# Kernel tuning notes

Hardware: AMD Instinct MI355X
Metric: run time of the kernel (lower is better)

The kernel has to match this reference:

```python
import jax, jax.numpy as jnp
import numpy as np

V, E, H = 512, 128, 256
B, S, T = 2048, 32, 48


def setup_inputs() -> dict:
    key = jax.random.key(0)
    ks = jax.random.split(key, 13)
    def p(i, shape):
        return jax.random.normal(ks[i], shape, dtype=jnp.float32) * 0.05
    return {
        "source": jax.random.randint(ks[0], (B, S), 0, V),
        "target_len": T,
        "enc_emb": p(1, (V, E)),
        "enc_Wih": p(2, (4 * H, E)),
        "enc_Whh": p(3, (4 * H, H)),
        "enc_bih": p(4, (4 * H,)),
        "enc_bhh": p(5, (4 * H,)),
        "dec_emb": p(6, (V, E)),
        "dec_Wih": p(7, (4 * H, E)),
        "dec_Whh": p(8, (4 * H, H)),
        "dec_bih": p(9, (4 * H,)),
        "dec_bhh": p(10, (4 * H,)),
        "fc_W": p(11, (V, H)),
        "fc_b": p(12, (V,)),
    }


def lstm_cell(x, h, c, Wih, Whh, bih, bhh):
    # torch gate order: i, f, g, o
    z = x @ Wih.T + h @ Whh.T + (bih + bhh)
    i, f, g, o = jnp.split(z, 4, axis=-1)
    c = jax.nn.sigmoid(f) * c + jax.nn.sigmoid(i) * jnp.tanh(g)
    h = jax.nn.sigmoid(o) * jnp.tanh(c)
    return h, c


def reference(source, target_len, enc_emb, enc_Wih, enc_Whh, enc_bih, enc_bhh,
              dec_emb, dec_Wih, dec_Whh, dec_bih, dec_bhh, fc_W, fc_b):
    Bsz = source.shape[0]
    Hd = enc_Whh.shape[1]
    h0 = jnp.zeros((Bsz, Hd), dtype=enc_emb.dtype)
    c0 = jnp.zeros((Bsz, Hd), dtype=enc_emb.dtype)

    # ---- encoder: embed whole source, scan single-layer LSTM over time ----
    emb_seq = jnp.swapaxes(enc_emb[source], 0, 1)  # [S, B, E]

    def enc_step(carry, x_t):
        h, c = carry
        h, c = lstm_cell(x_t, h, c, enc_Wih, enc_Whh, enc_bih, enc_bhh)
        return (h, c), None

    (h, c), _ = jax.lax.scan(enc_step, (h0, c0), emb_seq)

    sos = jnp.zeros((Bsz,), dtype=jnp.int32)  # char2idx.get('<SOS>', 0) == 0

    def dec_step(carry, _):
        tok, h, c = carry
        x = dec_emb[tok]                         # [B, E]
        h, c = lstm_cell(x, h, c, dec_Wih, dec_Whh, dec_bih, dec_bhh)
        logits = h @ fc_W.T + fc_b               # [B, V]
        nxt = jnp.argmax(logits, axis=-1).astype(jnp.int32)
        return (nxt, h, c), logits

    _, logits = jax.lax.scan(dec_step, (sos, h, c), None, length=target_len)
    return jnp.swapaxes(logits, 0, 1)            # [B, target_len, V]
```

## Files before the change

kernel.cpp:

```cpp
#include <hip/hip_runtime.h>
#include <cmath>

#define S_LEN 32
#define E_DIM 128
#define H_DIM 256
#define V_DIM 512
#define NTILE 12
#define W_TILES 8
#define TILE_SHORTS 8192
#define A_SHORTS 8192
#define ZPITCH 132

typedef _Float16 f16x8v __attribute__((ext_vector_type(8)));
typedef float f32x16 __attribute__((ext_vector_type(16)));

#define SCALE_S 4096.0f
#define INV_S   2.44140625e-4f

__device__ __forceinline__ float sigf(float x) { return 1.0f / (1.0f + expf(-x)); }

template<int L>
__device__ __forceinline__ unsigned short lvl_f16(float x) {
  _Float16 h1 = (_Float16)x;
  if (L == 1) return __builtin_bit_cast(unsigned short, h1);
  _Float16 h2 = (_Float16)((x - (float)h1) * SCALE_S);
  return __builtin_bit_cast(unsigned short, h2);
}

__global__ void prep_weights(const float* __restrict__ eemb, const float* __restrict__ demb,
                             const float* __restrict__ eWih, const float* __restrict__ eWhh,
                             const float* __restrict__ dWih, const float* __restrict__ dWhh,
                             unsigned short* __restrict__ We, unsigned short* __restrict__ Wd,
                             float* __restrict__ PE, float* __restrict__ PD,
                             float* __restrict__ h0, float* __restrict__ c,
                             int* __restrict__ tok)
{
  const int b = blockIdx.x;
  if (b >= 1152) {
    const int pb = b - 1152;
    const int gt = pb * 256 + threadIdx.x;
    float4 z = make_float4(0.f, 0.f, 0.f, 0.f);
    float4* p0 = (float4*)h0;
    float4* pc = (float4*)c;
    for (int i = gt; i < 131072; i += 16384) { p0[i] = z; pc[i] = z; }
    if (gt < 2048) tok[gt] = 0;
    return;
  }
  if (b >= 128) {
    const int pb  = b - 128;
    const int set = pb >> 9;
    const int v   = pb & 511;
    const float* Wih  = set ? dWih : eWih;
    const float* embr = (set ? demb : eemb) + (size_t)v * E_DIM;
    float* dst = (set ? PD : PE) + (size_t)v * 1024;
    const int n0 = threadIdx.x * 4;
    float acc[4] = {0.f, 0.f, 0.f, 0.f};
    #pragma unroll 4
    for (int k0 = 0; k0 < E_DIM; k0 += 4) {
      float4 e = *(const float4*)(embr + k0);
      #pragma unroll
      for (int i = 0; i < 4; ++i) {
        float4 wv = *(const float4*)(Wih + (size_t)(n0 + i) * E_DIM + k0);
        acc[i] = fmaf(e.x, wv.x, acc[i]);
        acc[i] = fmaf(e.y, wv.y, acc[i]);
        acc[i] = fmaf(e.z, wv.z, acc[i]);
        acc[i] = fmaf(e.w, wv.w, acc[i]);
      }
    }
    *(float4*)(dst + n0) = make_float4(acc[0], acc[1], acc[2], acc[3]);
    return;
  }
  const int j    = b % W_TILES;
  const int rest = b / W_TILES;
  const int nb   = rest & 7;
  const int set  = rest >> 3;
  const float* Whh = set ? dWhh : eWhh;
  unsigned short* dst = (set ? Wd : We) + ((size_t)nb * W_TILES + j) * TILE_SHORTS;
  const int lvl = (j < 4) ? 1 : 2;
  const int jj  = j & 3;

  for (int cpos = threadIdx.x; cpos < 1024; cpos += 256) {
    int fi = cpos >> 6, l = cpos & 63;
    int g = fi >> 2, kc = fi & 3;
    int n  = g * H_DIM + nb * 32 + (l & 31);
    int kk = jj * 64 + kc * 16 + (l >> 5) * 8;
    unsigned short o8[8];
    #pragma unroll
    for (int e = 0; e < 8; ++e) {
      float v = Whh[(size_t)n * H_DIM + kk + e];
      o8[e] = (lvl == 1) ? lvl_f16<1>(v) : lvl_f16<2>(v);
    }
    uint4 pk;
    pk.x = (unsigned)o8[0] | ((unsigned)o8[1] << 16);
    pk.y = (unsigned)o8[2] | ((unsigned)o8[3] << 16);
    pk.z = (unsigned)o8[4] | ((unsigned)o8[5] << 16);
    pk.w = (unsigned)o8[6] | ((unsigned)o8[7] << 16);
    *(uint4*)&dst[(size_t)cpos * 8] = pk;
  }
}

__device__ __forceinline__ void stage_A12(unsigned short* Ax1, unsigned short* Ax2,
                                          const float* __restrict__ hsrc,
                                          int arow, int q8) {
  #pragma unroll
  for (int j = 0; j < 8; ++j) {
    int kA = q8 * 4 + 32 * j;
    float4 v = *(const float4*)(hsrc + kA);
    _Float16 a1x = (_Float16)v.x, a1y = (_Float16)v.y,
             a1z = (_Float16)v.z, a1w = (_Float16)v.w;
    _Float16 a2x = (_Float16)((v.x - (float)a1x) * SCALE_S);
    _Float16 a2y = (_Float16)((v.y - (float)a1y) * SCALE_S);
    _Float16 a2z = (_Float16)((v.z - (float)a1z) * SCALE_S);
    _Float16 a2w = (_Float16)((v.w - (float)a1w) * SCALE_S);
    int lane_w = arow + ((kA >> 3) & 1) * 32;
    int idx = ((kA >> 4) * 64 + lane_w) * 8 + (kA & 7);
    uint2 p1, p2;
    p1.x = (unsigned)__builtin_bit_cast(unsigned short, a1x)
         | ((unsigned)__builtin_bit_cast(unsigned short, a1y) << 16);
    p1.y = (unsigned)__builtin_bit_cast(unsigned short, a1z)
         | ((unsigned)__builtin_bit_cast(unsigned short, a1w) << 16);
    p2.x = (unsigned)__builtin_bit_cast(unsigned short, a2x)
         | ((unsigned)__builtin_bit_cast(unsigned short, a2y) << 16);
    p2.y = (unsigned)__builtin_bit_cast(unsigned short, a2z)
         | ((unsigned)__builtin_bit_cast(unsigned short, a2w) << 16);
    *(uint2*)&Ax1[idx] = p1;
    *(uint2*)&Ax2[idx] = p2;
  }
}

__launch_bounds__(256, 2)
__global__ void lstm_mfma_kernel(const float* __restrict__ pcomp,
                                 const int* __restrict__ idx_src, int idx_stride, int idx_off,
                                 const unsigned short* __restrict__ Wf,
                                 const float* __restrict__ bih, const float* __restrict__ bhh,
                                 const float* __restrict__ h_in,
                                 float* __restrict__ h_out, float* __restrict__ c)
{
  __shared__ __align__(16) unsigned short smem[2 * A_SHORTS];
  unsigned short* Ax1 = smem;
  unsigned short* Ax2 = smem + A_SHORTS;

  const int tid  = threadIdx.x;
  const int lane = tid & 63;
  const int w    = tid >> 6;
  const int m0 = blockIdx.x * 32;
  const int nb = blockIdx.y;
  const int nc0 = nb * 32;

  const int arow = tid >> 3;
  const int q8   = tid & 7;
  const int token = idx_src[(size_t)(m0 + arow) * idx_stride + idx_off];
  const float* hsrc = h_in + (size_t)(m0 + arow) * H_DIM;

  const int col32 = lane & 31;
  const int lhi   = lane >> 5;

  const unsigned short* wbase = Wf + (size_t)nb * (W_TILES * TILE_SHORTS)
                                   + (size_t)(w * 4) * 512 + (size_t)lane * 8;

  f32x16 accA, accB;
  #pragma unroll
  for (int r = 0; r < 16; ++r) { accA[r] = 0.f; accB[r] = 0.f; }

  uint4 pA[4], pB[4], pC[4], pD[4];

#define LOADT(J, P)                                                            \
  {                                                                            \
    const unsigned short* bsrc = wbase + (size_t)((J) & 7) * TILE_SHORTS;      \
    _Pragma("unroll")                                                          \
    for (int kc = 0; kc < 4; ++kc) P[kc] = *(const uint4*)(bsrc + (size_t)kc * 512); \
  }

#define MFMAT(J, P, ACCX, AXB)                                                 \
  {                                                                            \
    _Pragma("unroll")                                                          \
    for (int kc = 0; kc < 4; ++kc) {                                           \
      f16x8v af = *(const f16x8v*)&AXB[(((J) & 3) * 4 + kc) * 512 + lane * 8]; \
      f16x8v bfr = __builtin_bit_cast(f16x8v, P[kc]);                          \
      ACCX = __builtin_amdgcn_mfma_f32_32x32x16_f16(af, bfr, ACCX, 0, 0, 0);   \
    }                                                                          \
  }

  LOADT(0, pA); LOADT(1, pB); LOADT(2, pC);

  stage_A12(Ax1, Ax2, hsrc, arow, q8);
  asm volatile("s_waitcnt lgkmcnt(0)" ::: "memory");
  __builtin_amdgcn_s_barrier();

  LOADT(3, pD);  MFMAT(0, pA, accA, Ax1);
  LOADT(4, pA);  MFMAT(1, pB, accA, Ax1);
  LOADT(5, pB);  MFMAT(2, pC, accA, Ax1);
  LOADT(6, pC);  MFMAT(3, pD, accA, Ax1);
  LOADT(7, pD);  MFMAT(4, pA, accB, Ax1);
  LOADT(8, pA);  MFMAT(5, pB, accB, Ax1);
  LOADT(9, pB);  MFMAT(6, pC, accB, Ax1);
  LOADT(10, pC); MFMAT(7, pD, accB, Ax1);
  LOADT(11, pD); MFMAT(8, pA, accB, Ax2);

  const int er = arow;
  const int ec = q8;
  const float* cp0 = c + (size_t)(m0 + er) * H_DIM + nc0 + ec * 4;
  float4 cold = *(const float4*)(cp0);
  const float* pxr = pcomp + (size_t)token * 1024 + nc0 + ec * 4;
  float pxa[4][4];
  #pragma unroll
  for (int g = 0; g < 4; ++g) {
    float4 t = *(const float4*)(pxr + g * H_DIM);
    pxa[g][0] = t.x; pxa[g][1] = t.y; pxa[g][2] = t.z; pxa[g][3] = t.w;
  }

  MFMAT(9, pB, accB, Ax2);
  MFMAT(10, pC, accB, Ax2);
  MFMAT(11, pD, accB, Ax2);

#undef LOADT
#undef MFMAT

  const float bsv = bih[w * H_DIM + nc0 + col32] + bhh[w * H_DIM + nc0 + col32];

  float* zb = (float*)smem;
  asm volatile("s_waitcnt lgkmcnt(0)" ::: "memory");
  __builtin_amdgcn_s_barrier();

  #pragma unroll
  for (int r = 0; r < 16; ++r) {
    int row_l = (r & 3) + 8 * (r >> 2) + 4 * lhi;
    zb[row_l * ZPITCH + col32 * 4 + w] = fmaf(accB[r], INV_S, accA[r]) + bsv;
  }

  asm volatile("s_waitcnt lgkmcnt(0)" ::: "memory");
  __builtin_amdgcn_s_barrier();

  {
    float* hp  = h_out + (size_t)(m0 + er) * H_DIM + nc0 + ec * 4;
    float* cpw = (float*)cp0;
    float cov[4] = {cold.x, cold.y, cold.z, cold.w};
    float cnv[4], hnv[4];
    #pragma unroll
    for (int cc = 0; cc < 4; ++cc) {
      float4 zq = *(const float4*)&zb[er * ZPITCH + (ec * 4 + cc) * 4];
      float zi = zq.x + pxa[0][cc];
      float zf = zq.y + pxa[1][cc];
      float zg = zq.z + pxa[2][cc];
      float zo = zq.w + pxa[3][cc];
      float cn = sigf(zf) * cov[cc] + sigf(zi) * tanhf(zg);
      cnv[cc] = cn;
      hnv[cc] = sigf(zo) * tanhf(cn);
    }
    *(float4*)cpw = make_float4(cnv[0], cnv[1], cnv[2], cnv[3]);
    *(float4*)hp  = make_float4(hnv[0], hnv[1], hnv[2], hnv[3]);
  }
}

__launch_bounds__(256)
__global__ void declog_kernel(const float* __restrict__ h,
                              const float* __restrict__ fcW,
                              const float* __restrict__ fcb,
                              float* __restrict__ out,
                              int* __restrict__ tok,
                              int t, int T)
{
  __shared__ float bv[8][256];
  __shared__ int   bi[8][256];

  const int tid  = threadIdx.x;
  const int lane = tid & 63;
  const int wv   = tid >> 6;
  const int r0   = blockIdx.x * 8;
  const int c0   = tid * 2;

  const float* hb  = h + (size_t)r0 * H_DIM;
  const float* w0p = fcW + (size_t)c0 * H_DIM;
  const float* w1p = w0p + H_DIM;

  float acc[8][2] = {};

  #pragma unroll 1
  for (int k0 = 0; k0 < H_DIM; k0 += 16) {
    float4 b0[4], b1[4];
    #pragma unroll
    for (int q = 0; q < 4; ++q) {
      b0[q] = *(const float4*)(w0p + k0 + q * 4);
      b1[q] = *(const float4*)(w1p + k0 + q * 4);
    }
    #pragma unroll
    for (int q = 0; q < 4; ++q) {
      #pragma unroll
      for (int r = 0; r < 8; ++r) {
        float4 a = *(const float4*)(hb + (size_t)r * H_DIM + k0 + q * 4);
        acc[r][0] = fmaf(a.x, b0[q].x, acc[r][0]);
        acc[r][0] = fmaf(a.y, b0[q].y, acc[r][0]);
        acc[r][0] = fmaf(a.z, b0[q].z, acc[r][0]);
        acc[r][0] = fmaf(a.w, b0[q].w, acc[r][0]);
        acc[r][1] = fmaf(a.x, b1[q].x, acc[r][1]);
        acc[r][1] = fmaf(a.y, b1[q].y, acc[r][1]);
        acc[r][1] = fmaf(a.z, b1[q].z, acc[r][1]);
        acc[r][1] = fmaf(a.w, b1[q].w, acc[r][1]);
      }
    }
  }

  const float fb0 = fcb[c0];
  const float fb1 = fcb[c0 + 1];
  #pragma unroll
  for (int r = 0; r < 8; ++r) {
    float z0 = acc[r][0] + fb0;
    float z1 = acc[r][1] + fb1;
    *(float2*)(out + (size_t)(r0 + r) * T * V_DIM + (size_t)t * V_DIM + c0)
        = make_float2(z0, z1);
    float v = z0; int ix = c0;
    if (z1 > v) { v = z1; ix = c0 + 1; }
    bv[r][tid] = v;
    bi[r][tid] = ix;
  }
  __syncthreads();

  #pragma unroll
  for (int rr = 0; rr < 2; ++rr) {
    int r = wv * 2 + rr;
    float best = bv[r][lane];
    int   bidx = bi[r][lane];
    #pragma unroll
    for (int s = 1; s < 4; ++s) {
      float ov = bv[r][lane + 64 * s];
      int   oi = bi[r][lane + 64 * s];
      if (ov > best || (ov == best && oi < bidx)) { best = ov; bidx = oi; }
    }
    #pragma unroll
    for (int off = 32; off; off >>= 1) {
      float ov = __shfl_xor(best, off);
      int   oi = __shfl_xor(bidx, off);
      if (ov > best || (ov == best && oi < bidx)) { best = ov; bidx = oi; }
    }
    if (lane == 0) tok[r0 + r] = bidx;
  }
}

extern "C" void kernel_launch(void* const* d_in, const int* in_sizes, int n_in,
                              void* d_out, int out_size, void* d_ws, size_t ws_size,
                              hipStream_t stream) {
  const int*   source  = (const int*)d_in[0];
  const float* enc_emb = (const float*)d_in[2];
  const float* enc_Wih = (const float*)d_in[3];
  const float* enc_Whh = (const float*)d_in[4];
  const float* enc_bih = (const float*)d_in[5];
  const float* enc_bhh = (const float*)d_in[6];
  const float* dec_emb = (const float*)d_in[7];
  const float* dec_Wih = (const float*)d_in[8];
  const float* dec_Whh = (const float*)d_in[9];
  const float* dec_bih = (const float*)d_in[10];
  const float* dec_bhh = (const float*)d_in[11];
  const float* fc_W    = (const float*)d_in[12];
  const float* fc_b    = (const float*)d_in[13];
  float* out = (float*)d_out;

  const int B = in_sizes[0] / S_LEN;
  const int T = out_size / (B * V_DIM);

  const size_t BH = (size_t)B * H_DIM;
  const size_t WFSZ = (size_t)8 * W_TILES * TILE_SHORTS;
  float* h0  = (float*)d_ws;
  float* h1  = h0 + BH;
  float* c   = h1 + BH;
  int*   tok = (int*)(c + BH);
  unsigned short* We = (unsigned short*)(tok + B);
  unsigned short* Wd = We + WFSZ;
  float* PE = (float*)(Wd + WFSZ);
  float* PD = PE + (size_t)V_DIM * 1024;

  prep_weights<<<dim3(128 + 1024 + 64), dim3(256), 0, stream>>>(
      enc_emb, dec_emb, enc_Wih, enc_Whh, dec_Wih, dec_Whh,
      We, Wd, PE, PD, h0, c, tok);

  dim3 blk(256);
  dim3 g_lstm(B / 32, H_DIM / 32);
  dim3 g_declog(B / 8);

  const float* hin = h0;
  float* hout = h1;

  for (int s = 0; s < S_LEN; ++s) {
    lstm_mfma_kernel<<<g_lstm, blk, 0, stream>>>(
        PE, source, S_LEN, s, We, enc_bih, enc_bhh, hin, hout, c);
    const float* tmp = hout; hout = (float*)hin; hin = tmp;
  }

  for (int t = 0; t < T; ++t) {
    lstm_mfma_kernel<<<g_lstm, blk, 0, stream>>>(
        PD, tok, 1, 0, Wd, dec_bih, dec_bhh, hin, hout, c);
    const float* tmp = hout; hout = (float*)hin; hin = tmp;
    declog_kernel<<<g_declog, blk, 0, stream>>>(hin, fc_W, fc_b, out, tok, t, T);
  }
}
```

Before: 1.679 ms.

## Fuse encoder and decoder steps into one persistent cooperative megakernel

Replaces the roughly 130 per-step kernel launches with a single persistent cooperative kernel of 512 blocks. Each group of 8 blocks sharing a 32-row batch slice synchronises through an atomic flag counter instead of kernel boundaries. The cell state now lives in registers across steps, and the logits/argmax stage runs inside the same kernel on 4 rows per block. The aim is to remove launch overhead and the global c round-trips, at the cost of spin-wait synchronisation, atomic loads of h, and reliance on all blocks being co-resident.

```diff
diff --git a/kernel.cpp b/kernel.cpp
--- a/kernel.cpp
+++ b/kernel.cpp
@@ -27,23 +27,55 @@
   return __builtin_bit_cast(unsigned short, h2);
 }
 
+__device__ __forceinline__ float4 aload4(const float* p) {
+  const unsigned long long* q = (const unsigned long long*)p;
+  unsigned long long u0 = __hip_atomic_load(q,     __ATOMIC_RELAXED, __HIP_MEMORY_SCOPE_AGENT);
+  unsigned long long u1 = __hip_atomic_load(q + 1, __ATOMIC_RELAXED, __HIP_MEMORY_SCOPE_AGENT);
+  float4 v;
+  v.x = __uint_as_float((unsigned)u0); v.y = __uint_as_float((unsigned)(u0 >> 32));
+  v.z = __uint_as_float((unsigned)u1); v.w = __uint_as_float((unsigned)(u1 >> 32));
+  return v;
+}
+__device__ __forceinline__ void astore4(float* p, float4 v) {
+  unsigned long long u0 = (unsigned long long)__float_as_uint(v.x)
+                        | ((unsigned long long)__float_as_uint(v.y) << 32);
+  unsigned long long u1 = (unsigned long long)__float_as_uint(v.z)
+                        | ((unsigned long long)__float_as_uint(v.w) << 32);
+  __hip_atomic_store((unsigned long long*)p,     u0, __ATOMIC_RELAXED, __HIP_MEMORY_SCOPE_AGENT);
+  __hip_atomic_store((unsigned long long*)p + 1, u1, __ATOMIC_RELAXED, __HIP_MEMORY_SCOPE_AGENT);
+}
+
+__device__ __forceinline__ void group_wait(int* flag, int target) {
+  if (threadIdx.x == 0) {
+    while (__hip_atomic_load(flag, __ATOMIC_ACQUIRE, __HIP_MEMORY_SCOPE_AGENT) < target)
+      __builtin_amdgcn_s_sleep(2);
+  }
+  __syncthreads();
+}
+__device__ __forceinline__ void group_arrive(int* flag) {
+  __syncthreads();
+  if (threadIdx.x == 0)
+    __hip_atomic_fetch_add(flag, 1, __ATOMIC_RELEASE, __HIP_MEMORY_SCOPE_AGENT);
+}
+
 __global__ void prep_weights(const float* __restrict__ eemb, const float* __restrict__ demb,
                              const float* __restrict__ eWih, const float* __restrict__ eWhh,
                              const float* __restrict__ dWih, const float* __restrict__ dWhh,
                              unsigned short* __restrict__ We, unsigned short* __restrict__ Wd,
                              float* __restrict__ PE, float* __restrict__ PD,
-                             float* __restrict__ h0, float* __restrict__ c,
-                             int* __restrict__ tok)
+                             float* __restrict__ hB, float* __restrict__ c,
+                             int* __restrict__ tok, int* __restrict__ flags)
 {
   const int b = blockIdx.x;
   if (b >= 1152) {
     const int pb = b - 1152;
     const int gt = pb * 256 + threadIdx.x;
     float4 z = make_float4(0.f, 0.f, 0.f, 0.f);
-    float4* p0 = (float4*)h0;
+    float4* p0 = (float4*)hB;
     float4* pc = (float4*)c;
     for (int i = gt; i < 131072; i += 16384) { p0[i] = z; pc[i] = z; }
     if (gt < 2048) tok[gt] = 0;
+    if (gt < 64) flags[gt] = 0;
     return;
   }
   if (b >= 128) {
@@ -96,6 +128,34 @@
     pk.z = (unsigned)o8[4] | ((unsigned)o8[5] << 16);
     pk.w = (unsigned)o8[6] | ((unsigned)o8[7] << 16);
     *(uint4*)&dst[(size_t)cpos * 8] = pk;
+  }
+}
+
+__device__ __forceinline__ void stage_A12m(unsigned short* Ax1, unsigned short* Ax2,
+                                           const float* hsrc, int arow, int q8) {
+  #pragma unroll
+  for (int j = 0; j < 8; ++j) {
+    int kA = q8 * 4 + 32 * j;
+    float4 v = aload4(hsrc + kA);
+    _Float16 a1x = (_Float16)v.x, a1y = (_Float16)v.y,
+             a1z = (_Float16)v.z, a1w = (_Float16)v.w;
+    _Float16 a2x = (_Float16)((v.x - (float)a1x) * SCALE_S);
+    _Float16 a2y = (_Float16)((v.y - (float)a1y) * SCALE_S);
+    _Float16 a2z = (_Float16)((v.z - (float)a1z) * SCALE_S);
+    _Float16 a2w = (_Float16)((v.w - (float)a1w) * SCALE_S);
+    int lane_w = arow + ((kA >> 3) & 1) * 32;
+    int idx = ((kA >> 4) * 64 + lane_w) * 8 + (kA & 7);
+    uint2 p1, p2;
+    p1.x = (unsigned)__builtin_bit_cast(unsigned short, a1x)
+         | ((unsigned)__builtin_bit_cast(unsigned short, a1y) << 16);
+    p1.y = (unsigned)__builtin_bit_cast(unsigned short, a1z)
+         | ((unsigned)__builtin_bit_cast(unsigned short, a1w) << 16);
+    p2.x = (unsigned)__builtin_bit_cast(unsigned short, a2x)
+         | ((unsigned)__builtin_bit_cast(unsigned short, a2y) << 16);
+    p2.y = (unsigned)__builtin_bit_cast(unsigned short, a2z)
+         | ((unsigned)__builtin_bit_cast(unsigned short, a2w) << 16);
+    *(uint2*)&Ax1[idx] = p1;
+    *(uint2*)&Ax2[idx] = p2;
   }
 }
 
@@ -128,6 +188,227 @@
   }
 }
 
+#define LOADT(J, P)                                                            \
+  {                                                                            \
+    const unsigned short* bsrc = wb + (size_t)((J) & 7) * TILE_SHORTS;         \
+    _Pragma("unroll")                                                          \
+    for (int kc = 0; kc < 4; ++kc) P[kc] = *(const uint4*)(bsrc + (size_t)kc * 512); \
+  }
+
+#define MFMAT(J, P, ACCX, AXB)                                                 \
+  {                                                                            \
+    _Pragma("unroll")                                                          \
+    for (int kc = 0; kc < 4; ++kc) {                                           \
+      f16x8v af = *(const f16x8v*)&AXB[(((J) & 3) * 4 + kc) * 512 + lane * 8]; \
+      f16x8v bfr = __builtin_bit_cast(f16x8v, P[kc]);                          \
+      ACCX = __builtin_amdgcn_mfma_f32_32x32x16_f16(af, bfr, ACCX, 0, 0, 0);   \
+    }                                                                          \
+  }
+
+__launch_bounds__(256, 2)
+__global__ void seq2seq_mega(
+    const int* __restrict__ source,
+    const float* __restrict__ PE, const float* __restrict__ PD,
+    const unsigned short* __restrict__ We, const unsigned short* __restrict__ Wd,
+    const float* __restrict__ ebih, const float* __restrict__ ebhh,
+    const float* __restrict__ dbih, const float* __restrict__ dbhh,
+    const float* __restrict__ fcW, const float* __restrict__ fcb,
+    float* __restrict__ out, float* __restrict__ hA, float* __restrict__ hB,
+    int* __restrict__ tok, int* __restrict__ flags, int T)
+{
+  __shared__ __align__(16) unsigned short smem[2 * A_SHORTS];
+  unsigned short* Ax1 = smem;
+  unsigned short* Ax2 = smem + A_SHORTS;
+
+  const int tid  = threadIdx.x;
+  const int lane = tid & 63;
+  const int w    = tid >> 6;
+  const int bid  = blockIdx.x;
+  const int g    = bid & 63;
+  const int nb   = bid >> 6;
+  const int m0   = g * 32;
+  const int nc0  = nb * 32;
+  int* flag = &flags[g];
+  int E = 0;
+
+  const int arow = tid >> 3;
+  const int q8   = tid & 7;
+  const int col32 = lane & 31;
+  const int lhi   = lane >> 5;
+
+  const float ebs = ebih[w * H_DIM + nc0 + col32] + ebhh[w * H_DIM + nc0 + col32];
+  const float dbs = dbih[w * H_DIM + nc0 + col32] + dbhh[w * H_DIM + nc0 + col32];
+
+  float c_reg[4] = {0.f, 0.f, 0.f, 0.f};
+
+  const int nsteps = S_LEN + T;
+  for (int s = 0; s < nsteps; ++s) {
+    const bool enc = (s < S_LEN);
+
+    group_wait(flag, 8 * E);
+
+    int token;
+    if (enc)            token = source[(size_t)(m0 + arow) * S_LEN + s];
+    else if (s == S_LEN) token = 0;
+    else                 token = __hip_atomic_load(&tok[m0 + arow], __ATOMIC_RELAXED,
+                                                   __HIP_MEMORY_SCOPE_AGENT);
+
+    const float* hprev = (s & 1) ? hA : hB;
+    const float* hsrc  = hprev + (size_t)(m0 + arow) * H_DIM;
+    const unsigned short* wb = (enc ? We : Wd) + (size_t)nb * (W_TILES * TILE_SHORTS)
+                             + (size_t)(w * 4) * 512 + (size_t)lane * 8;
+
+    f32x16 accA, accB;
+    #pragma unroll
+    for (int r = 0; r < 16; ++r) { accA[r] = 0.f; accB[r] = 0.f; }
+
+    uint4 pA[4], pB[4], pC[4], pD[4];
+
+    LOADT(0, pA); LOADT(1, pB); LOADT(2, pC);
+
+    stage_A12m(Ax1, Ax2, hsrc, arow, q8);
+    asm volatile("s_waitcnt lgkmcnt(0)" ::: "memory");
+    __builtin_amdgcn_s_barrier();
+
+    LOADT(3, pD);  MFMAT(0, pA, accA, Ax1);
+    LOADT(4, pA);  MFMAT(1, pB, accA, Ax1);
+    LOADT(5, pB);  MFMAT(2, pC, accA, Ax1);
+    LOADT(6, pC);  MFMAT(3, pD, accA, Ax1);
+    LOADT(7, pD);  MFMAT(4, pA, accB, Ax1);
+    LOADT(8, pA);  MFMAT(5, pB, accB, Ax1);
+    LOADT(9, pB);  MFMAT(6, pC, accB, Ax1);
+    LOADT(10, pC); MFMAT(7, pD, accB, Ax1);
+    LOADT(11, pD); MFMAT(8, pA, accB, Ax2);
+
+    const float* pxr = (enc ? PE : PD) + (size_t)token * 1024 + nc0 + q8 * 4;
+    float pxa[4][4];
+    #pragma unroll
+    for (int gg = 0; gg < 4; ++gg) {
+      float4 t = *(const float4*)(pxr + gg * H_DIM);
+      pxa[gg][0] = t.x; pxa[gg][1] = t.y; pxa[gg][2] = t.z; pxa[gg][3] = t.w;
+    }
+
+    MFMAT(9, pB, accB, Ax2);
+    MFMAT(10, pC, accB, Ax2);
+    MFMAT(11, pD, accB, Ax2);
+
+    const float bsv = enc ? ebs : dbs;
+    float* zb = (float*)smem;
+    asm volatile("s_waitcnt lgkmcnt(0)" ::: "memory");
+    __builtin_amdgcn_s_barrier();
+
+    #pragma unroll
+    for (int r = 0; r < 16; ++r) {
+      int row_l = (r & 3) + 8 * (r >> 2) + 4 * lhi;
+      zb[row_l * ZPITCH + col32 * 4 + w] = fmaf(accB[r], INV_S, accA[r]) + bsv;
+    }
+    asm volatile("s_waitcnt lgkmcnt(0)" ::: "memory");
+    __builtin_amdgcn_s_barrier();
+
+    {
+      float* hcur = ((s & 1) ? hB : hA) + (size_t)(m0 + arow) * H_DIM + nc0 + q8 * 4;
+      float hnv[4];
+      #pragma unroll
+      for (int cc = 0; cc < 4; ++cc) {
+        float4 zq = *(const float4*)&zb[arow * ZPITCH + (q8 * 4 + cc) * 4];
+        float zi = zq.x + pxa[0][cc];
+        float zf = zq.y + pxa[1][cc];
+        float zg = zq.z + pxa[2][cc];
+        float zo = zq.w + pxa[3][cc];
+        float cn = sigf(zf) * c_reg[cc] + sigf(zi) * tanhf(zg);
+        c_reg[cc] = cn;
+        hnv[cc] = sigf(zo) * tanhf(cn);
+      }
+      astore4(hcur, make_float4(hnv[0], hnv[1], hnv[2], hnv[3]));
+    }
+    group_arrive(flag); ++E;
+
+    if (!enc) {
+      const int t = s - S_LEN;
+      group_wait(flag, 8 * E);
+
+      const int r0d = m0 + nb * 4;
+      const float* hnow = (s & 1) ? hB : hA;
+      float (*dAs)[260] = (float (*)[260])smem;
+      float (*bv)[256]  = (float (*)[256])((char*)smem + 17408);
+      int   (*bi)[256]  = (int (*)[256])((char*)smem + 21504);
+
+      {
+        int srow = tid >> 6;
+        int scol = (tid & 63) * 4;
+        float4 hv4 = aload4(hnow + (size_t)(r0d + srow) * H_DIM + scol);
+        *(float4*)&dAs[srow][scol] = hv4;
+      }
+      __syncthreads();
+
+      const int c0 = tid * 2;
+      const float* w0p = fcW + (size_t)c0 * H_DIM;
+      const float* w1p = w0p + H_DIM;
+      float acc[4][2] = {};
+
+      #pragma unroll 1
+      for (int k0 = 0; k0 < H_DIM; k0 += 16) {
+        float4 b0[4], b1[4];
+        #pragma unroll
+        for (int q = 0; q < 4; ++q) {
+          b0[q] = *(const float4*)(w0p + k0 + q * 4);
+          b1[q] = *(const float4*)(w1p + k0 + q * 4);
+        }
+        #pragma unroll
+        for (int q = 0; q < 4; ++q) {
+          #pragma unroll
+          for (int r = 0; r < 4; ++r) {
+            float4 a = *(const float4*)&dAs[r][k0 + q * 4];
+            acc[r][0] = fmaf(a.x, b0[q].x, acc[r][0]);
+            acc[r][0] = fmaf(a.y, b0[q].y, acc[r][0]);
+            acc[r][0] = fmaf(a.z, b0[q].z, acc[r][0]);
+            acc[r][0] = fmaf(a.w, b0[q].w, acc[r][0]);
+            acc[r][1] = fmaf(a.x, b1[q].x, acc[r][1]);
+            acc[r][1] = fmaf(a.y, b1[q].y, acc[r][1]);
+            acc[r][1] = fmaf(a.z, b1[q].z, acc[r][1]);
+            acc[r][1] = fmaf(a.w, b1[q].w, acc[r][1]);
+          }
+        }
+      }
+
+      const float fb0 = fcb[c0];
+      const float fb1 = fcb[c0 + 1];
+      #pragma unroll
+      for (int r = 0; r < 4; ++r) {
+        float z0 = acc[r][0] + fb0;
+        float z1 = acc[r][1] + fb1;
+        *(float2*)(out + ((size_t)(r0d + r) * T + t) * V_DIM + c0) = make_float2(z0, z1);
+        float v = z0; int ix = c0;
+        if (z1 > v) { v = z1; ix = c0 + 1; }
+        bv[r][tid] = v;
+        bi[r][tid] = ix;
+      }
+      __syncthreads();
+
+      {
+        const int wv = w;
+        float best = bv[wv][lane];
+        int   bidx = bi[wv][lane];
+        #pragma unroll
+        for (int ss = 1; ss < 4; ++ss) {
+          float ov = bv[wv][lane + 64 * ss];
+          int   oi = bi[wv][lane + 64 * ss];
+          if (ov > best || (ov == best && oi < bidx)) { best = ov; bidx = oi; }
+        }
+        #pragma unroll
+        for (int off = 32; off; off >>= 1) {
+          float ov = __shfl_xor(best, off);
+          int   oi = __shfl_xor(bidx, off);
+          if (ov > best || (ov == best && oi < bidx)) { best = ov; bidx = oi; }
+        }
+        if (lane == 0)
+          __hip_atomic_store(&tok[r0d + wv], bidx, __ATOMIC_RELAXED, __HIP_MEMORY_SCOPE_AGENT);
+      }
+      group_arrive(flag); ++E;
+    }
+  }
+}
+
 __launch_bounds__(256, 2)
 __global__ void lstm_mfma_kernel(const float* __restrict__ pcomp,
                                  const int* __restrict__ idx_src, int idx_stride, int idx_off,
@@ -151,12 +432,11 @@
   const int q8   = tid & 7;
   const int token = idx_src[(size_t)(m0 + arow) * idx_stride + idx_off];
   const float* hsrc = h_in + (size_t)(m0 + arow) * H_DIM;
-
   const int col32 = lane & 31;
   const int lhi   = lane >> 5;
 
-  const unsigned short* wbase = Wf + (size_t)nb * (W_TILES * TILE_SHORTS)
-                                   + (size_t)(w * 4) * 512 + (size_t)lane * 8;
+  const unsigned short* wb = Wf + (size_t)nb * (W_TILES * TILE_SHORTS)
+                           + (size_t)(w * 4) * 512 + (size_t)lane * 8;
 
   f32x16 accA, accB;
   #pragma unroll
@@ -164,25 +444,7 @@
 
   uint4 pA[4], pB[4], pC[4], pD[4];
 
-#define LOADT(J, P)                                                            \
-  {                                                                            \
-    const unsigned short* bsrc = wbase + (size_t)((J) & 7) * TILE_SHORTS;      \
-    _Pragma("unroll")                                                          \
-    for (int kc = 0; kc < 4; ++kc) P[kc] = *(const uint4*)(bsrc + (size_t)kc * 512); \
-  }
-
-#define MFMAT(J, P, ACCX, AXB)                                                 \
-  {                                                                            \
-    _Pragma("unroll")                                                          \
-    for (int kc = 0; kc < 4; ++kc) {                                           \
-      f16x8v af = *(const f16x8v*)&AXB[(((J) & 3) * 4 + kc) * 512 + lane * 8]; \
-      f16x8v bfr = __builtin_bit_cast(f16x8v, P[kc]);                          \
-      ACCX = __builtin_amdgcn_mfma_f32_32x32x16_f16(af, bfr, ACCX, 0, 0, 0);   \
-    }                                                                          \
-  }
-
   LOADT(0, pA); LOADT(1, pB); LOADT(2, pC);
-
   stage_A12(Ax1, Ax2, hsrc, arow, q8);
   asm volatile("s_waitcnt lgkmcnt(0)" ::: "memory");
   __builtin_amdgcn_s_barrier();
@@ -197,48 +459,39 @@
   LOADT(10, pC); MFMAT(7, pD, accB, Ax1);
   LOADT(11, pD); MFMAT(8, pA, accB, Ax2);
 
-  const int er = arow;
-  const int ec = q8;
-  const float* cp0 = c + (size_t)(m0 + er) * H_DIM + nc0 + ec * 4;
+  const float* cp0 = c + (size_t)(m0 + arow) * H_DIM + nc0 + q8 * 4;
   float4 cold = *(const float4*)(cp0);
-  const float* pxr = pcomp + (size_t)token * 1024 + nc0 + ec * 4;
+  const float* pxr = pcomp + (size_t)token * 1024 + nc0 + q8 * 4;
   float pxa[4][4];
   #pragma unroll
-  for (int g = 0; g < 4; ++g) {
-    float4 t = *(const float4*)(pxr + g * H_DIM);
-    pxa[g][0] = t.x; pxa[g][1] = t.y; pxa[g][2] = t.z; pxa[g][3] = t.w;
+  for (int gg = 0; gg < 4; ++gg) {
+    float4 t = *(const float4*)(pxr + gg * H_DIM);
+    pxa[gg][0] = t.x; pxa[gg][1] = t.y; pxa[gg][2] = t.z; pxa[gg][3] = t.w;
   }
 
   MFMAT(9, pB, accB, Ax2);
   MFMAT(10, pC, accB, Ax2);
   MFMAT(11, pD, accB, Ax2);
 
-#undef LOADT
-#undef MFMAT
-
   const float bsv = bih[w * H_DIM + nc0 + col32] + bhh[w * H_DIM + nc0 + col32];
-
   float* zb = (float*)smem;
   asm volatile("s_waitcnt lgkmcnt(0)" ::: "memory");
   __builtin_amdgcn_s_barrier();
-
   #pragma unroll
   for (int r = 0; r < 16; ++r) {
     int row_l = (r & 3) + 8 * (r >> 2) + 4 * lhi;
     zb[row_l * ZPITCH + col32 * 4 + w] = fmaf(accB[r], INV_S, accA[r]) + bsv;
   }
-
   asm volatile("s_waitcnt lgkmcnt(0)" ::: "memory");
   __builtin_amdgcn_s_barrier();
-
   {
-    float* hp  = h_out + (size_t)(m0 + er) * H_DIM + nc0 + ec * 4;
+    float* hp  = h_out + (size_t)(m0 + arow) * H_DIM + nc0 + q8 * 4;
     float* cpw = (float*)cp0;
     float cov[4] = {cold.x, cold.y, cold.z, cold.w};
     float cnv[4], hnv[4];
     #pragma unroll
     for (int cc = 0; cc < 4; ++cc) {
-      float4 zq = *(const float4*)&zb[er * ZPITCH + (ec * 4 + cc) * 4];
+      float4 zq = *(const float4*)&zb[arow * ZPITCH + (q8 * 4 + cc) * 4];
       float zi = zq.x + pxa[0][cc];
       float zf = zq.y + pxa[1][cc];
       float zg = zq.z + pxa[2][cc];
@@ -253,28 +506,21 @@
 }
 
 __launch_bounds__(256)
-__global__ void declog_kernel(const float* __restrict__ h,
-                              const float* __restrict__ fcW,
-                              const float* __restrict__ fcb,
-                              float* __restrict__ out,
-                              int* __restrict__ tok,
-                              int t, int T)
+__global__ void declog_kernel(const float* __restrict__ h, const float* __restrict__ fcW,
+                              const float* __restrict__ fcb, float* __restrict__ out,
+                              int* __restrict__ tok, int t, int T)
 {
   __shared__ float bv[8][256];
   __shared__ int   bi[8][256];
-
   const int tid  = threadIdx.x;
   const int lane = tid & 63;
   const int wv   = tid >> 6;
   const int r0   = blockIdx.x * 8;
   const int c0   = tid * 2;
-
   const float* hb  = h + (size_t)r0 * H_DIM;
   const float* w0p = fcW + (size_t)c0 * H_DIM;
   const float* w1p = w0p + H_DIM;
-
   float acc[8][2] = {};
-
   #pragma unroll 1
   for (int k0 = 0; k0 < H_DIM; k0 += 16) {
     float4 b0[4], b1[4];
@@ -299,31 +545,28 @@
       }
     }
   }
-
   const float fb0 = fcb[c0];
   const float fb1 = fcb[c0 + 1];
   #pragma unroll
   for (int r = 0; r < 8; ++r) {
     float z0 = acc[r][0] + fb0;
     float z1 = acc[r][1] + fb1;
-    *(float2*)(out + (size_t)(r0 + r) * T * V_DIM + (size_t)t * V_DIM + c0)
-        = make_float2(z0, z1);
+    *(float2*)(out + (size_t)(r0 + r) * T * V_DIM + (size_t)t * V_DIM + c0) = make_float2(z0, z1);
     float v = z0; int ix = c0;
     if (z1 > v) { v = z1; ix = c0 + 1; }
     bv[r][tid] = v;
     bi[r][tid] = ix;
   }
   __syncthreads();
-
   #pragma unroll
   for (int rr = 0; rr < 2; ++rr) {
     int r = wv * 2 + rr;
     float best = bv[r][lane];
     int   bidx = bi[r][lane];
     #pragma unroll
-    for (int s = 1; s < 4; ++s) {
-      float ov = bv[r][lane + 64 * s];
-      int   oi = bi[r][lane + 64 * s];
+    for (int ss = 1; ss < 4; ++ss) {
+      float ov = bv[r][lane + 64 * ss];
+      int   oi = bi[r][lane + 64 * ss];
       if (ov > best || (ov == best && oi < bidx)) { best = ov; bidx = oi; }
     }
     #pragma unroll
@@ -355,40 +598,53 @@
   float* out = (float*)d_out;
 
   const int B = in_sizes[0] / S_LEN;
-  const int T = out_size / (B * V_DIM);
+  int T = out_size / (B * V_DIM);
 
   const size_t BH = (size_t)B * H_DIM;
   const size_t WFSZ = (size_t)8 * W_TILES * TILE_SHORTS;
-  float* h0  = (float*)d_ws;
-  float* h1  = h0 + BH;
-  float* c   = h1 + BH;
+  float* hA  = (float*)d_ws;
+  float* hB  = hA + BH;
+  float* c   = hB + BH;
   int*   tok = (int*)(c + BH);
-  unsigned short* We = (unsigned short*)(tok + B);
+  int*   flags = tok + B;
+  unsigned short* We = (unsigned short*)(flags + 64);
   unsigned short* Wd = We + WFSZ;
   float* PE = (float*)(Wd + WFSZ);
   float* PD = PE + (size_t)V_DIM * 1024;
 
   prep_weights<<<dim3(128 + 1024 + 64), dim3(256), 0, stream>>>(
       enc_emb, dec_emb, enc_Wih, enc_Whh, dec_Wih, dec_Whh,
-      We, Wd, PE, PD, h0, c, tok);
-
-  dim3 blk(256);
-  dim3 g_lstm(B / 32, H_DIM / 32);
-  dim3 g_declog(B / 8);
-
-  const float* hin = h0;
-  float* hout = h1;
-
-  for (int s = 0; s < S_LEN; ++s) {
-    lstm_mfma_kernel<<<g_lstm, blk, 0, stream>>>(
-        PE, source, S_LEN, s, We, enc_bih, enc_bhh, hin, hout, c);
-    const float* tmp = hout; hout = (float*)hin; hin = tmp;
-  }
-
-  for (int t = 0; t < T; ++t) {
-    lstm_mfma_kernel<<<g_lstm, blk, 0, stream>>>(
-        PD, tok, 1, 0, Wd, dec_bih, dec_bhh, hin, hout, c);
-    const float* tmp = hout; hout = (float*)hin; hin = tmp;
-    declog_kernel<<<g_declog, blk, 0, stream>>>(hin, fc_W, fc_b, out, tok, t, T);
-  }
-}
+      We, Wd, PE, PD, hB, c, tok, flags);
+
+  int nblk = 0;
+  hipOccupancyMaxActiveBlocksPerMultiprocessor(&nblk,
+      reinterpret_cast<const void*>(&seq2seq_mega), 256, 0);
+
+  if (nblk >= 2) {
+    void* args[] = {
+      (void*)&source, (void*)&PE, (void*)&PD, (void*)&We, (void*)&Wd,
+      (void*)&enc_bih, (void*)&enc_bhh, (void*)&dec_bih, (void*)&dec_bhh,
+      (void*)&fc_W, (void*)&fc_b,
+      (void*)&out, (void*)&hA, (void*)&hB, (void*)&tok, (void*)&flags, (void*)&T
+    };
+    hipLaunchCooperativeKernel(reinterpret_cast<const void*>(&seq2seq_mega),
+                               dim3(512), dim3(256), args, 0, stream);
+  } else {
+    dim3 blk(256);
+    dim3 g_lstm(B / 32, H_DIM / 32);
+    dim3 g_declog(B / 8);
+    const float* hin = hB;
+    float* hout = hA;
+    for (int s = 0; s < S_LEN; ++s) {
+      lstm_mfma_kernel<<<g_lstm, blk, 0, stream>>>(
+          PE, source, S_LEN, s, We, enc_bih, enc_bhh, hin, hout, c);
+      const float* tmp = hout; hout = (float*)hin; hin = tmp;
+    }
+    for (int t = 0; t < T; ++t) {
+      lstm_mfma_kernel<<<g_lstm, blk, 0, stream>>>(
+          PD, tok, 1, 0, Wd, dec_bih, dec_bhh, hin, hout, c);
+      const float* tmp = hout; hout = (float*)hin; hin = tmp;
+      declog_kernel<<<g_declog, blk, 0, stream>>>(hin, fc_W, fc_b, out, tok, t, T);
+    }
+  }
+}
```

After: 1.680 ms. About the same (+0.1%).
